# Kernel tuning notes

Hardware: AMD Instinct MI355X
Metric: run time of the kernel (lower is better)

Reference implementation:

```python
import jax, jax.numpy as jnp
import numpy as np

D = 256  # atom_feature_dim
LN_EPS = 1e-5
NEG_SLOPE = 0.01  # LeakyReLU default


def setup_inputs() -> dict:
    key = jax.random.key(0)
    ks = jax.random.split(key, 8)
    B, N, L = 16, 256, 1024
    inv = 1.0 / np.sqrt(D)
    return {
        "mol_atom_feature": jax.random.normal(ks[0], (B, N, D), jnp.float32),
        "atom_feature": jax.random.normal(ks[1], (B, L, D), jnp.float32),
        "mol_atom_attend_mask": jnp.ones((B, L), jnp.float32),
        "mol_atom_softmax_mask": jnp.zeros((B, L), jnp.float32),
        # nn.Linear(D, D) params (weight stored [out, in] torch-style; we use x @ W.T form via einsum)
        "W_mol": jax.random.uniform(ks[2], (D, D), jnp.float32, -inv, inv),
        "b_mol": jnp.zeros((D,), jnp.float32),
        "W_nb": jax.random.uniform(ks[3], (D, D), jnp.float32, -inv, inv),
        "b_nb": jnp.zeros((D,), jnp.float32),
        # nn.Linear(2D, 1): weight [2D], bias scalar
        "align_w": jax.random.uniform(ks[4], (2 * D,), jnp.float32, -1.0 / np.sqrt(2 * D), 1.0 / np.sqrt(2 * D)),
        "align_b": jnp.zeros((), jnp.float32),
        "ln_gamma": jnp.ones((D,), jnp.float32),
        "ln_beta": jnp.zeros((D,), jnp.float32),
    }


def reference(mol_atom_feature, atom_feature, mol_atom_attend_mask, mol_atom_softmax_mask,
              W_mol, b_mol, W_nb, b_nb, align_w, align_b, ln_gamma, ln_beta):
    # Linear transforms (dropout is identity in eval)
    x = jnp.einsum('bnd,ed->bne', mol_atom_feature, W_mol) + b_mol   # [B,N,D]
    a = jnp.einsum('bld,ed->ble', atom_feature, W_nb) + b_nb        # [B,L,D]

    # GAT align: Linear over concat([x_i, a_j]) is separable:
    # score[b,n,l] = x[b,n]@w1 + a[b,l]@w2 + b
    w1, w2 = align_w[:D], align_w[D:]
    score = (x @ w1)[:, :, None] + (a @ w2)[:, None, :] + align_b   # [B,N,L]
    score = jax.nn.leaky_relu(score, NEG_SLOPE)

    # additive softmax mask over atom axis, then masked softmax + attend mask
    score = score + mol_atom_softmax_mask[:, None, :]
    attn = jax.nn.softmax(score, axis=-1)
    attn = attn * mol_atom_attend_mask[:, None, :]

    # weighted aggregation of transformed atom features
    ctx = jnp.einsum('bnl,bld->bnd', attn, a)                        # [B,N,D]

    # LayerNorm
    mu = jnp.mean(ctx, axis=-1, keepdims=True)
    var = jnp.var(ctx, axis=-1, keepdims=True)
    out = (ctx - mu) * jax.lax.rsqrt(var + LN_EPS) * ln_gamma + ln_beta
    return out
```

## Files before the change

kernel.cpp:

```cpp
#include <hip/hip_runtime.h>
#include <hip/hip_bf16.h>
#include <math.h>

#define BB 16
#define NN 256
#define LL 1024
#define DD 256

constexpr float LN_EPS = 1e-5f;
constexpr float NEG_SLOPE = 0.01f;

typedef __attribute__((ext_vector_type(8))) short short8;
typedef __attribute__((ext_vector_type(4))) float f32x4;
typedef __attribute__((ext_vector_type(4))) int i32x4;

static __device__ __forceinline__ unsigned cvtpk(float lo, float hi) {
  __hip_bfloat162 h = __float22bfloat162_rn(make_float2(lo, hi));
  union { __hip_bfloat162 h; unsigned u; } v; v.h = h;
  return v.u;
}
static __device__ __forceinline__ short8 pack8(float4 f0, float4 f1) {
  union { i32x4 i; short8 s; } v;
  v.i.x = cvtpk(f0.x, f0.y);
  v.i.y = cvtpk(f0.z, f0.w);
  v.i.z = cvtpk(f1.x, f1.y);
  v.i.w = cvtpk(f1.z, f1.w);
  return v.s;
}
static __device__ __forceinline__ unsigned short f2bf(float f) {
  union { float f; unsigned u; } v; v.f = f;
  unsigned r = v.u + 0x7FFFu + ((v.u >> 16) & 1u);
  return (unsigned short)(r >> 16);
}
static __device__ __forceinline__ float bf2f(unsigned short u) {
  union { unsigned u; float f; } v; v.u = ((unsigned)u) << 16;
  return v.f;
}

__global__ __launch_bounds__(1024) void agemm_kernel(
    const float* __restrict__ atom, const float* __restrict__ W_nb,
    const float* __restrict__ b_nb, const float* __restrict__ W_mol,
    const float* __restrict__ b_mol, const float* __restrict__ align_w,
    const float* __restrict__ align_b, unsigned short* __restrict__ aT,
    float* __restrict__ s2, float* __restrict__ v1c) {
  __shared__ char atile[64 * 256 * 2];
  __shared__ unsigned short sAT[256 * 68];
  __shared__ float vp[64][16];

  int t = threadIdx.x;
  int w = t >> 6, lane = t & 63;
  int i = blockIdx.x;
  int x = i & 7, k = i >> 3;
  int b = x + 8 * (k >> 4);
  int l0 = (k & 15) * 64;
  int lo16 = lane & 15, g = lane >> 4;

  {
    int r = t >> 4, dseg = (t & 15) * 16;
    const float* src = atom + (size_t)(b * LL + l0 + r) * DD + dseg;
    #pragma unroll
    for (int q = 0; q < 2; ++q) {
      float4 f0 = *(const float4*)(src + q * 8);
      float4 f1 = *(const float4*)(src + q * 8 + 4);
      int byte = ((r * 256 + dseg + q * 8) * 2) ^ ((r & 7) << 4);
      *(short8*)(atile + byte) = pack8(f0, f1);
    }
  }

  if (i < 16) {
    int d0 = i * 16;
    int dl = t & 15, eseg = t >> 4;
    float acc = 0.f;
    #pragma unroll
    for (int q = 0; q < 4; ++q) {
      int e = eseg * 4 + q;
      acc += align_w[e] * W_mol[e * DD + d0 + dl];
    }
    vp[eseg][dl] = acc;
    __syncthreads();
    if (t < 16) {
      float s = 0.f;
      #pragma unroll
      for (int q = 0; q < 64; ++q) s += vp[q][t];
      v1c[d0 + t] = s;
    }
    if (i == 0 && w == 1) {
      float s = b_mol[lane] * align_w[lane] +
                b_mol[lane + 64] * align_w[lane + 64] +
                b_mol[lane + 128] * align_w[lane + 128] +
                b_mol[lane + 192] * align_w[lane + 192];
      #pragma unroll
      for (int off = 32; off > 0; off >>= 1) s += __shfl_xor(s, off, 64);
      if (lane == 0) v1c[256] = s + align_b[0];
    }
  }
  __syncthreads();

  f32x4 acc[4];
  #pragma unroll
  for (int n = 0; n < 4; ++n) acc[n] = f32x4{0.f, 0.f, 0.f, 0.f};

  const float* Ap = W_nb + (size_t)(w * 16 + lo16) * DD + g * 8;

  #pragma unroll 4
  for (int kk = 0; kk < 8; ++kk) {
    float4 f0 = *(const float4*)(Ap + kk * 32);
    float4 f1 = *(const float4*)(Ap + kk * 32 + 4);
    short8 af = pack8(f0, f1);
    #pragma unroll
    for (int n = 0; n < 4; ++n) {
      int l = n * 16 + lo16;
      int byte = ((l * 256 + kk * 32 + g * 8) * 2) ^ ((l & 7) << 4);
      short8 bf = *(const short8*)(atile + byte);
      acc[n] = __builtin_amdgcn_mfma_f32_16x16x32_bf16(af, bf, acc[n], 0, 0, 0);
    }
  }

  {
    int e_lo = w * 16 + g * 4;
    float4 bias = *(const float4*)&b_nb[e_lo];
    #pragma unroll
    for (int n = 0; n < 4; ++n) {
      int l = n * 16 + lo16;
      #pragma unroll
      for (int j = 0; j < 4; ++j) {
        float v = acc[n][j] + ((const float*)&bias)[j];
        sAT[(e_lo + j) * 68 + l] = f2bf(v);
      }
    }
  }
  __syncthreads();

  {
    int l = t >> 4, ech = (t & 15) * 16;
    float s = 0.f;
    #pragma unroll 8
    for (int q = 0; q < 16; ++q) {
      int e = ech + q;
      s += align_w[DD + e] * bf2f(sAT[e * 68 + l]);
    }
    s += __shfl_xor(s, 1, 64);
    s += __shfl_xor(s, 2, 64);
    s += __shfl_xor(s, 4, 64);
    s += __shfl_xor(s, 8, 64);
    if ((t & 15) == 0) s2[b * LL + l0 + l] = s;
  }

  unsigned short* dst = aT + (size_t)b * DD * LL + l0;
  #pragma unroll
  for (int idx = t; idx < 4096; idx += 1024) {
    int e = idx >> 4, ch = idx & 15;
    ushort4 v = *(const ushort4*)&sAT[e * 68 + ch * 4];
    *(ushort4*)(dst + (size_t)e * LL + ch * 4) = v;
  }
}

__global__ __launch_bounds__(1024) void attn_kernel(
    const unsigned short* __restrict__ aT, const float* __restrict__ mol,
    const float* __restrict__ v1c, const float* __restrict__ s2,
    const float* __restrict__ amask, const float* __restrict__ smask,
    const float* __restrict__ gamma, const float* __restrict__ beta,
    float* __restrict__ out) {
  __shared__ unsigned short sattn[16 * 1024];
  __shared__ float ctxp[4][16][DD];
  __shared__ float v1s[256];
  __shared__ float s1s[16];
  __shared__ float mu_s[16], rs_s[16];
  int i = blockIdx.x;
  int x = i & 7, k = i >> 3;
  int b = x + 8 * (k >> 4);
  int n0 = (k & 15) * 16;
  int t = threadIdx.x, w = t >> 6, lane = t & 63;

  float c0 = v1c[256];
  if (t < 256) v1s[t] = v1c[t];
  __syncthreads();

  {
    const float* mr = mol + (size_t)(b * NN + n0 + w) * DD + lane * 4;
    float4 f = *(const float4*)mr;
    float s = f.x * v1s[lane * 4] + f.y * v1s[lane * 4 + 1] +
              f.z * v1s[lane * 4 + 2] + f.w * v1s[lane * 4 + 3];
    #pragma unroll
    for (int off = 32; off > 0; off >>= 1) s += __shfl_xor(s, off, 64);
    if (lane == 0) s1s[w] = s + c0;
  }
  __syncthreads();

  {
    int r = w;
    float s1v = s1s[r];
    float p[16], amv[16];
    float mx = -INFINITY;
    #pragma unroll
    for (int q = 0; q < 16; ++q) {
      int l = lane + 64 * q;
      float sc = s1v + s2[b * LL + l];
      sc = sc > 0.f ? sc : NEG_SLOPE * sc;
      sc += smask[b * LL + l];
      amv[q] = amask[b * LL + l];
      p[q] = sc;
      mx = fmaxf(mx, sc);
    }
    #pragma unroll
    for (int off = 32; off > 0; off >>= 1) mx = fmaxf(mx, __shfl_xor(mx, off, 64));
    float sum = 0.f;
    #pragma unroll
    for (int q = 0; q < 16; ++q) {
      p[q] = __expf(p[q] - mx);
      sum += p[q];
    }
    #pragma unroll
    for (int off = 32; off > 0; off >>= 1) sum += __shfl_xor(sum, off, 64);
    float inv = 1.f / sum;
    #pragma unroll
    for (int q = 0; q < 16; ++q) {
      unsigned short bv = f2bf(p[q] * amv[q] * inv);
      int l = lane + 64 * q;
      int byte = ((r * 1024 + l) * 2) ^ ((r & 7) << 4);
      *(unsigned short*)((char*)sattn + byte) = bv;
    }
  }
  __syncthreads();

  int lo16 = lane & 15, g = lane >> 4;
  int e0 = (w & 3) * 64, lq = w >> 2;
  f32x4 acc[4];
  #pragma unroll
  for (int n = 0; n < 4; ++n) acc[n] = f32x4{0.f, 0.f, 0.f, 0.f};
  const unsigned short* Bp =
      aT + (size_t)b * DD * LL + (size_t)(e0 + lo16) * LL + lq * 256 + g * 8;
  #pragma unroll 4
  for (int kk = 0; kk < 8; ++kk) {
    short8 afr = *(const short8*)((const char*)sattn +
        (((lo16 * 1024 + lq * 256 + kk * 32 + g * 8) * 2) ^ ((lo16 & 7) << 4)));
    #pragma unroll
    for (int n = 0; n < 4; ++n) {
      short8 bfr = *(const short8*)(Bp + (size_t)n * 16 * LL + kk * 32);
      acc[n] = __builtin_amdgcn_mfma_f32_16x16x32_bf16(afr, bfr, acc[n], 0, 0, 0);
    }
  }
  #pragma unroll
  for (int n = 0; n < 4; ++n)
    #pragma unroll
    for (int j = 0; j < 4; ++j)
      ctxp[lq][g * 4 + j][e0 + n * 16 + lo16] = acc[n][j];
  __syncthreads();

  {
    int r = w;
    float s = 0.f, sq = 0.f;
    #pragma unroll
    for (int jj = 0; jj < 4; ++jj) {
      int cc = lane + 64 * jj;
      float v = ctxp[0][r][cc] + ctxp[1][r][cc] + ctxp[2][r][cc] + ctxp[3][r][cc];
      s += v;
      sq += v * v;
    }
    #pragma unroll
    for (int off = 32; off > 0; off >>= 1) {
      s += __shfl_xor(s, off, 64);
      sq += __shfl_xor(sq, off, 64);
    }
    if (lane == 0) {
      float mu = s * (1.f / 256.f);
      float var = sq * (1.f / 256.f) - mu * mu;
      mu_s[r] = mu;
      rs_s[r] = rsqrtf(var + LN_EPS);
    }
  }
  __syncthreads();

  #pragma unroll
  for (int q = 0; q < 4; ++q) {
    int idx = t + 1024 * q;
    int r = idx >> 8, d = idx & 255;
    float v = ctxp[0][r][d] + ctxp[1][r][d] + ctxp[2][r][d] + ctxp[3][r][d];
    out[(size_t)(b * NN + n0 + r) * DD + d] =
        (v - mu_s[r]) * rs_s[r] * gamma[d] + beta[d];
  }
}

extern "C" void kernel_launch(void* const* d_in, const int* in_sizes, int n_in,
                              void* d_out, int out_size, void* d_ws, size_t ws_size,
                              hipStream_t stream) {
  const float* mol     = (const float*)d_in[0];
  const float* atom    = (const float*)d_in[1];
  const float* amask   = (const float*)d_in[2];
  const float* smask   = (const float*)d_in[3];
  const float* W_mol   = (const float*)d_in[4];
  const float* b_mol   = (const float*)d_in[5];
  const float* W_nb    = (const float*)d_in[6];
  const float* b_nb    = (const float*)d_in[7];
  const float* align_w = (const float*)d_in[8];
  const float* align_b = (const float*)d_in[9];
  const float* gamma   = (const float*)d_in[10];
  const float* beta    = (const float*)d_in[11];
  float* outp = (float*)d_out;

  char* wsb = (char*)d_ws;
  unsigned short* aT = (unsigned short*)wsb;
  float* s2  = (float*)(wsb + 8388608);
  float* v1c = s2 + BB * LL;

  agemm_kernel<<<256, 1024, 0, stream>>>(atom, W_nb, b_nb, W_mol, b_mol,
                                         align_w, align_b, aT, s2, v1c);
  attn_kernel<<<256, 1024, 0, stream>>>(aT, mol, v1c, s2, amask, smask,
                                        gamma, beta, outp);
}
```

Baseline: 41.66 us.

## Fuse projection and attention kernels with per-batch atomic barrier

Merges the two launches into one kernel. Each block computes its 64-row slice of the atom projection, then waits on a per-batch atomic counter until all 16 blocks of that batch are done before running attention. Every block now recomputes the v1 vector (W_mol^T w1) redundantly, and the masks and s2 are staged in shared memory. This removes a kernel launch and its gap but adds a memset launch and relies on all 256 blocks being co-resident; otherwise the spin-wait can deadlock.

```diff
diff --git a/kernel.cpp b/kernel.cpp
--- a/kernel.cpp
+++ b/kernel.cpp
@@ -37,22 +37,38 @@
   return v.f;
 }
 
-__global__ __launch_bounds__(1024) void agemm_kernel(
-    const float* __restrict__ atom, const float* __restrict__ W_nb,
-    const float* __restrict__ b_nb, const float* __restrict__ W_mol,
-    const float* __restrict__ b_mol, const float* __restrict__ align_w,
-    const float* __restrict__ align_b, unsigned short* __restrict__ aT,
-    float* __restrict__ s2, float* __restrict__ v1c) {
-  __shared__ char atile[64 * 256 * 2];
-  __shared__ unsigned short sAT[256 * 68];
-  __shared__ float vp[64][16];
-
-  int t = threadIdx.x;
-  int w = t >> 6, lane = t & 63;
+struct P1 {
+  char atile[64 * 256 * 2];
+  unsigned short sAT[256 * 68];
+  float vp[4][256];
+};
+struct P2 {
+  unsigned short sattn[16 * 1024];
+  float ctxp[4][16][DD];
+};
+
+__global__ __launch_bounds__(1024, 4) void fused_kernel(
+    const float* __restrict__ mol, const float* __restrict__ atom,
+    const float* __restrict__ amask, const float* __restrict__ smask,
+    const float* __restrict__ W_mol, const float* __restrict__ b_mol,
+    const float* __restrict__ W_nb, const float* __restrict__ b_nb,
+    const float* __restrict__ align_w, const float* __restrict__ align_b,
+    const float* __restrict__ gamma, const float* __restrict__ beta,
+    unsigned short* __restrict__ aT, float* __restrict__ s2g,
+    unsigned int* __restrict__ cnt, float* __restrict__ outp) {
+  __shared__ union { P1 p1; P2 p2; } sh;
+  __shared__ float am_s[LL], sm_s[LL], s2_s[LL];
+  __shared__ float v1s[256];
+  __shared__ float s1s[16], mu_s[16], rs_s[16];
+  __shared__ float c0s;
+
+  int t = threadIdx.x, w = t >> 6, lane = t & 63;
   int i = blockIdx.x;
   int x = i & 7, k = i >> 3;
   int b = x + 8 * (k >> 4);
-  int l0 = (k & 15) * 64;
+  int j = k & 15;
+  int l0 = j * 64;
+  int n0 = j * 16;
   int lo16 = lane & 15, g = lane >> 4;
 
   {
@@ -63,69 +79,64 @@
       float4 f0 = *(const float4*)(src + q * 8);
       float4 f1 = *(const float4*)(src + q * 8 + 4);
       int byte = ((r * 256 + dseg + q * 8) * 2) ^ ((r & 7) << 4);
-      *(short8*)(atile + byte) = pack8(f0, f1);
-    }
-  }
-
-  if (i < 16) {
-    int d0 = i * 16;
-    int dl = t & 15, eseg = t >> 4;
+      *(short8*)(sh.p1.atile + byte) = pack8(f0, f1);
+    }
+  }
+  if (t < 256) {
+    *(float4*)&am_s[t * 4] = *(const float4*)&amask[b * LL + t * 4];
+  } else if (t < 512) {
+    int u = t - 256;
+    *(float4*)&sm_s[u * 4] = *(const float4*)&smask[b * LL + u * 4];
+  }
+  {
+    int d = t & 255, eq = t >> 8;
     float acc = 0.f;
-    #pragma unroll
-    for (int q = 0; q < 4; ++q) {
-      int e = eseg * 4 + q;
-      acc += align_w[e] * W_mol[e * DD + d0 + dl];
-    }
-    vp[eseg][dl] = acc;
-    __syncthreads();
-    if (t < 16) {
-      float s = 0.f;
+    #pragma unroll 8
+    for (int e = eq * 64; e < eq * 64 + 64; ++e)
+      acc += align_w[e] * W_mol[e * DD + d];
+    sh.p1.vp[eq][d] = acc;
+  }
+  __syncthreads();
+
+  if (t < 256)
+    v1s[t] = sh.p1.vp[0][t] + sh.p1.vp[1][t] + sh.p1.vp[2][t] + sh.p1.vp[3][t];
+  if (w == 15) {
+    float s = b_mol[lane] * align_w[lane] +
+              b_mol[lane + 64] * align_w[lane + 64] +
+              b_mol[lane + 128] * align_w[lane + 128] +
+              b_mol[lane + 192] * align_w[lane + 192];
+    #pragma unroll
+    for (int off = 32; off > 0; off >>= 1) s += __shfl_xor(s, off, 64);
+    if (lane == 0) c0s = s + align_b[0];
+  }
+
+  {
+    f32x4 acc[4];
+    #pragma unroll
+    for (int n = 0; n < 4; ++n) acc[n] = f32x4{0.f, 0.f, 0.f, 0.f};
+    const float* Ap = W_nb + (size_t)(w * 16 + lo16) * DD + g * 8;
+    #pragma unroll 4
+    for (int kk = 0; kk < 8; ++kk) {
+      float4 f0 = *(const float4*)(Ap + kk * 32);
+      float4 f1 = *(const float4*)(Ap + kk * 32 + 4);
+      short8 af = pack8(f0, f1);
       #pragma unroll
-      for (int q = 0; q < 64; ++q) s += vp[q][t];
-      v1c[d0 + t] = s;
-    }
-    if (i == 0 && w == 1) {
-      float s = b_mol[lane] * align_w[lane] +
-                b_mol[lane + 64] * align_w[lane + 64] +
-                b_mol[lane + 128] * align_w[lane + 128] +
-                b_mol[lane + 192] * align_w[lane + 192];
-      #pragma unroll
-      for (int off = 32; off > 0; off >>= 1) s += __shfl_xor(s, off, 64);
-      if (lane == 0) v1c[256] = s + align_b[0];
-    }
-  }
-  __syncthreads();
-
-  f32x4 acc[4];
-  #pragma unroll
-  for (int n = 0; n < 4; ++n) acc[n] = f32x4{0.f, 0.f, 0.f, 0.f};
-
-  const float* Ap = W_nb + (size_t)(w * 16 + lo16) * DD + g * 8;
-
-  #pragma unroll 4
-  for (int kk = 0; kk < 8; ++kk) {
-    float4 f0 = *(const float4*)(Ap + kk * 32);
-    float4 f1 = *(const float4*)(Ap + kk * 32 + 4);
-    short8 af = pack8(f0, f1);
-    #pragma unroll
-    for (int n = 0; n < 4; ++n) {
-      int l = n * 16 + lo16;
-      int byte = ((l * 256 + kk * 32 + g * 8) * 2) ^ ((l & 7) << 4);
-      short8 bf = *(const short8*)(atile + byte);
-      acc[n] = __builtin_amdgcn_mfma_f32_16x16x32_bf16(af, bf, acc[n], 0, 0, 0);
-    }
-  }
-
-  {
+      for (int n = 0; n < 4; ++n) {
+        int l = n * 16 + lo16;
+        int byte = ((l * 256 + kk * 32 + g * 8) * 2) ^ ((l & 7) << 4);
+        short8 bf = *(const short8*)(sh.p1.atile + byte);
+        acc[n] = __builtin_amdgcn_mfma_f32_16x16x32_bf16(af, bf, acc[n], 0, 0, 0);
+      }
+    }
     int e_lo = w * 16 + g * 4;
     float4 bias = *(const float4*)&b_nb[e_lo];
     #pragma unroll
     for (int n = 0; n < 4; ++n) {
       int l = n * 16 + lo16;
       #pragma unroll
-      for (int j = 0; j < 4; ++j) {
-        float v = acc[n][j] + ((const float*)&bias)[j];
-        sAT[(e_lo + j) * 68 + l] = f2bf(v);
+      for (int jj = 0; jj < 4; ++jj) {
+        float v = acc[n][jj] + ((const float*)&bias)[jj];
+        sh.p1.sAT[(e_lo + jj) * 68 + l] = f2bf(v);
       }
     }
   }
@@ -137,45 +148,23 @@
     #pragma unroll 8
     for (int q = 0; q < 16; ++q) {
       int e = ech + q;
-      s += align_w[DD + e] * bf2f(sAT[e * 68 + l]);
+      s += align_w[DD + e] * bf2f(sh.p1.sAT[e * 68 + l]);
     }
     s += __shfl_xor(s, 1, 64);
     s += __shfl_xor(s, 2, 64);
     s += __shfl_xor(s, 4, 64);
     s += __shfl_xor(s, 8, 64);
-    if ((t & 15) == 0) s2[b * LL + l0 + l] = s;
-  }
-
-  unsigned short* dst = aT + (size_t)b * DD * LL + l0;
-  #pragma unroll
-  for (int idx = t; idx < 4096; idx += 1024) {
-    int e = idx >> 4, ch = idx & 15;
-    ushort4 v = *(const ushort4*)&sAT[e * 68 + ch * 4];
-    *(ushort4*)(dst + (size_t)e * LL + ch * 4) = v;
-  }
-}
-
-__global__ __launch_bounds__(1024) void attn_kernel(
-    const unsigned short* __restrict__ aT, const float* __restrict__ mol,
-    const float* __restrict__ v1c, const float* __restrict__ s2,
-    const float* __restrict__ amask, const float* __restrict__ smask,
-    const float* __restrict__ gamma, const float* __restrict__ beta,
-    float* __restrict__ out) {
-  __shared__ unsigned short sattn[16 * 1024];
-  __shared__ float ctxp[4][16][DD];
-  __shared__ float v1s[256];
-  __shared__ float s1s[16];
-  __shared__ float mu_s[16], rs_s[16];
-  int i = blockIdx.x;
-  int x = i & 7, k = i >> 3;
-  int b = x + 8 * (k >> 4);
-  int n0 = (k & 15) * 16;
-  int t = threadIdx.x, w = t >> 6, lane = t & 63;
-
-  float c0 = v1c[256];
-  if (t < 256) v1s[t] = v1c[t];
-  __syncthreads();
-
+    if ((t & 15) == 0) s2g[b * LL + l0 + l] = s;
+  }
+  {
+    unsigned short* dst = aT + (size_t)b * DD * LL + l0;
+    #pragma unroll
+    for (int idx = t; idx < 4096; idx += 1024) {
+      int e = idx >> 4, ch = idx & 15;
+      ushort4 v = *(const ushort4*)&sh.p1.sAT[e * 68 + ch * 4];
+      *(ushort4*)(dst + (size_t)e * LL + ch * 4) = v;
+    }
+  }
   {
     const float* mr = mol + (size_t)(b * NN + n0 + w) * DD + lane * 4;
     float4 f = *(const float4*)mr;
@@ -183,22 +172,35 @@
               f.z * v1s[lane * 4 + 2] + f.w * v1s[lane * 4 + 3];
     #pragma unroll
     for (int off = 32; off > 0; off >>= 1) s += __shfl_xor(s, off, 64);
-    if (lane == 0) s1s[w] = s + c0;
-  }
+    if (lane == 0) s1s[w] = s + c0s;
+  }
+  __syncthreads();
+
+  if (t == 0) {
+    __threadfence();
+    atomicAdd(&cnt[b], 1u);
+    while (__hip_atomic_load(&cnt[b], __ATOMIC_ACQUIRE,
+                             __HIP_MEMORY_SCOPE_AGENT) < 16u) {
+      __builtin_amdgcn_s_sleep(2);
+    }
+    __threadfence();
+  }
+  __syncthreads();
+
+  if (t < 256) *(float4*)&s2_s[t * 4] = *(const float4*)&s2g[b * LL + t * 4];
   __syncthreads();
 
   {
     int r = w;
     float s1v = s1s[r];
-    float p[16], amv[16];
+    float p[16];
     float mx = -INFINITY;
     #pragma unroll
     for (int q = 0; q < 16; ++q) {
       int l = lane + 64 * q;
-      float sc = s1v + s2[b * LL + l];
+      float sc = s1v + s2_s[l];
       sc = sc > 0.f ? sc : NEG_SLOPE * sc;
-      sc += smask[b * LL + l];
-      amv[q] = amask[b * LL + l];
+      sc += sm_s[l];
       p[q] = sc;
       mx = fmaxf(mx, sc);
     }
@@ -215,36 +217,37 @@
     float inv = 1.f / sum;
     #pragma unroll
     for (int q = 0; q < 16; ++q) {
-      unsigned short bv = f2bf(p[q] * amv[q] * inv);
       int l = lane + 64 * q;
+      unsigned short bv = f2bf(p[q] * am_s[l] * inv);
       int byte = ((r * 1024 + l) * 2) ^ ((r & 7) << 4);
-      *(unsigned short*)((char*)sattn + byte) = bv;
-    }
-  }
-  __syncthreads();
-
-  int lo16 = lane & 15, g = lane >> 4;
-  int e0 = (w & 3) * 64, lq = w >> 2;
-  f32x4 acc[4];
-  #pragma unroll
-  for (int n = 0; n < 4; ++n) acc[n] = f32x4{0.f, 0.f, 0.f, 0.f};
-  const unsigned short* Bp =
-      aT + (size_t)b * DD * LL + (size_t)(e0 + lo16) * LL + lq * 256 + g * 8;
-  #pragma unroll 4
-  for (int kk = 0; kk < 8; ++kk) {
-    short8 afr = *(const short8*)((const char*)sattn +
-        (((lo16 * 1024 + lq * 256 + kk * 32 + g * 8) * 2) ^ ((lo16 & 7) << 4)));
-    #pragma unroll
-    for (int n = 0; n < 4; ++n) {
-      short8 bfr = *(const short8*)(Bp + (size_t)n * 16 * LL + kk * 32);
-      acc[n] = __builtin_amdgcn_mfma_f32_16x16x32_bf16(afr, bfr, acc[n], 0, 0, 0);
-    }
-  }
-  #pragma unroll
-  for (int n = 0; n < 4; ++n)
-    #pragma unroll
-    for (int j = 0; j < 4; ++j)
-      ctxp[lq][g * 4 + j][e0 + n * 16 + lo16] = acc[n][j];
+      *(unsigned short*)((char*)sh.p2.sattn + byte) = bv;
+    }
+  }
+  __syncthreads();
+
+  {
+    int e0 = (w & 3) * 64, lq = w >> 2;
+    f32x4 acc[4];
+    #pragma unroll
+    for (int n = 0; n < 4; ++n) acc[n] = f32x4{0.f, 0.f, 0.f, 0.f};
+    const unsigned short* Bp =
+        aT + (size_t)b * DD * LL + (size_t)(e0 + lo16) * LL + lq * 256 + g * 8;
+    #pragma unroll 4
+    for (int kk = 0; kk < 8; ++kk) {
+      short8 afr = *(const short8*)((const char*)sh.p2.sattn +
+          (((lo16 * 1024 + lq * 256 + kk * 32 + g * 8) * 2) ^ ((lo16 & 7) << 4)));
+      #pragma unroll
+      for (int n = 0; n < 4; ++n) {
+        short8 bfr = *(const short8*)(Bp + (size_t)n * 16 * LL + kk * 32);
+        acc[n] = __builtin_amdgcn_mfma_f32_16x16x32_bf16(afr, bfr, acc[n], 0, 0, 0);
+      }
+    }
+    #pragma unroll
+    for (int n = 0; n < 4; ++n)
+      #pragma unroll
+      for (int jj = 0; jj < 4; ++jj)
+        sh.p2.ctxp[lq][g * 4 + jj][e0 + n * 16 + lo16] = acc[n][jj];
+  }
   __syncthreads();
 
   {
@@ -253,7 +256,8 @@
     #pragma unroll
     for (int jj = 0; jj < 4; ++jj) {
       int cc = lane + 64 * jj;
-      float v = ctxp[0][r][cc] + ctxp[1][r][cc] + ctxp[2][r][cc] + ctxp[3][r][cc];
+      float v = sh.p2.ctxp[0][r][cc] + sh.p2.ctxp[1][r][cc] +
+                sh.p2.ctxp[2][r][cc] + sh.p2.ctxp[3][r][cc];
       s += v;
       sq += v * v;
     }
@@ -275,8 +279,9 @@
   for (int q = 0; q < 4; ++q) {
     int idx = t + 1024 * q;
     int r = idx >> 8, d = idx & 255;
-    float v = ctxp[0][r][d] + ctxp[1][r][d] + ctxp[2][r][d] + ctxp[3][r][d];
-    out[(size_t)(b * NN + n0 + r) * DD + d] =
+    float v = sh.p2.ctxp[0][r][d] + sh.p2.ctxp[1][r][d] +
+              sh.p2.ctxp[2][r][d] + sh.p2.ctxp[3][r][d];
+    outp[(size_t)(b * NN + n0 + r) * DD + d] =
         (v - mu_s[r]) * rs_s[r] * gamma[d] + beta[d];
   }
 }
@@ -300,11 +305,11 @@
 
   char* wsb = (char*)d_ws;
   unsigned short* aT = (unsigned short*)wsb;
-  float* s2  = (float*)(wsb + 8388608);
-  float* v1c = s2 + BB * LL;
-
-  agemm_kernel<<<256, 1024, 0, stream>>>(atom, W_nb, b_nb, W_mol, b_mol,
-                                         align_w, align_b, aT, s2, v1c);
-  attn_kernel<<<256, 1024, 0, stream>>>(aT, mol, v1c, s2, amask, smask,
-                                        gamma, beta, outp);
-}
+  float* s2g = (float*)(wsb + 8388608);
+  unsigned int* cnt = (unsigned int*)(wsb + 8388608 + 65536);
+
+  hipMemsetAsync(cnt, 0, 16 * sizeof(unsigned int), stream);
+  fused_kernel<<<256, 1024, 0, stream>>>(mol, atom, amask, smask, W_mol, b_mol,
+                                         W_nb, b_nb, align_w, align_b, gamma,
+                                         beta, aT, s2g, cnt, outp);
+}
```

After: 72.68 us. 1.74x slower.
